# Kernel optimization log

Hardware: AMD Instinct MI355X
Metric: run time of the kernel (lower is better)

Reference implementation:

```python
import jax, jax.numpy as jnp
import numpy as np

B, S, D = 4, 4096, 1024

def setup_inputs() -> dict:
    key = jax.random.key(0)
    ks = jax.random.split(key, 7)
    scale = 1.0 / np.sqrt(D)
    X  = jax.random.normal(ks[0], (B, S, D), dtype=jnp.float32)
    Wq = jax.random.normal(ks[1], (D, D), dtype=jnp.float32) * scale
    bq = jnp.zeros((D,), dtype=jnp.float32)
    Wk = jax.random.normal(ks[2], (D, D), dtype=jnp.float32) * scale
    bk = jnp.zeros((D,), dtype=jnp.float32)
    Wv = jax.random.normal(ks[3], (D, D), dtype=jnp.float32) * scale
    bv = jnp.zeros((D,), dtype=jnp.float32)
    return {"X": X, "Wq": Wq, "bq": bq, "Wk": Wk, "bk": bk, "Wv": Wv, "bv": bv}

def reference(X, Wq, bq, Wk, bk, Wv, bv):
    # Linear projections (torch Linear: x @ W.T + b; here W stored as [D_in, D_out])
    Q = jnp.einsum('bsd,de->bse', X, Wq) + bq
    K = jnp.einsum('bsd,de->bse', X, Wk) + bk
    V = jnp.einsum('bsd,de->bse', X, Wv) + bv
    inv_sqrt_d = 1.0 / jnp.sqrt(jnp.float32(X.shape[-1]))
    scores = jnp.einsum('bqd,bkd->bqk', Q, K) * inv_sqrt_d  # [B,S,S]
    weights = jax.nn.sigmoid(scores)  # elementwise, no row normalization
    return jnp.einsum('bqk,bkd->bqd', weights, V)
```

## Files before the change

kernel.cpp:

```cpp
#include <hip/hip_runtime.h>
#include <hip/hip_bf16.h>

typedef __bf16 bf16_t;
typedef bf16_t bf16x8 __attribute__((ext_vector_type(8)));
typedef float f32x4 __attribute__((ext_vector_type(4)));

constexpr int D_DIM = 1024;
constexpr int S_DIM = 4096;
constexpr int B_DIM = 4;

__global__ void cast_f32_bf16(const float* __restrict__ in, bf16_t* __restrict__ out) {
  size_t i = ((size_t)blockIdx.x * blockDim.x + threadIdx.x) * 8;
  float4 a = *(const float4*)(in + i);
  float4 b = *(const float4*)(in + i + 4);
  bf16x8 o;
  o[0] = (bf16_t)a.x; o[1] = (bf16_t)a.y; o[2] = (bf16_t)a.z; o[3] = (bf16_t)a.w;
  o[4] = (bf16_t)b.x; o[5] = (bf16_t)b.y; o[6] = (bf16_t)b.z; o[7] = (bf16_t)b.w;
  *(bf16x8*)(out + i) = o;
}

__global__ void transpose_cast_1024(const float* __restrict__ in, bf16_t* __restrict__ out) {
  __shared__ float t[32][33];
  int x0 = blockIdx.x * 32, y0 = blockIdx.y * 32;
#pragma unroll
  for (int i = 0; i < 32; i += 8)
    t[threadIdx.y + i][threadIdx.x] =
        in[(size_t)(y0 + threadIdx.y + i) * D_DIM + (x0 + threadIdx.x)];
  __syncthreads();
#pragma unroll
  for (int i = 0; i < 32; i += 8)
    out[(size_t)(x0 + threadIdx.y + i) * D_DIM + (y0 + threadIdx.x)] =
        (bf16_t)t[threadIdx.x][threadIdx.y + i];
}

constexpr int BM2 = 256, BN2 = 256;

#define VMCNT4 asm volatile("s_waitcnt vmcnt(4)" ::: "memory")
#define VMCNT0 asm volatile("s_waitcnt vmcnt(0)" ::: "memory")
#define CFENCE asm volatile("" ::: "memory")
#define BAR __builtin_amdgcn_s_barrier()
#define PRIO1 __builtin_amdgcn_s_setprio(1)
#define PRIO0 __builtin_amdgcn_s_setprio(0)

__device__ __forceinline__ void stage_half(const bf16_t* __restrict__ g, int ld,
                                           char* lds, int tid) {
  const int w = tid >> 6, l = tid & 63;
  const int rw = l >> 3;
  const int gl = (l & 7) ^ rw;
  char* l0 = lds + w * 1024;
  const bf16_t* s0 = g + (size_t)(w * 8 + rw) * ld + gl * 8;
  __builtin_amdgcn_global_load_lds((const __attribute__((address_space(1))) void*)s0,
                                   (__attribute__((address_space(3))) void*)l0, 16, 0, 0);
  __builtin_amdgcn_global_load_lds(
      (const __attribute__((address_space(1))) void*)(s0 + (size_t)64 * ld),
      (__attribute__((address_space(3))) void*)(l0 + 8192), 16, 0, 0);
}

__device__ __forceinline__ void load_a4(const char* __restrict__ At, int wr, int fm, int s,
                                        int kxa, int kxb, bf16x8 (&af)[4][2]) {
#pragma unroll
  for (int m = 0; m < 4; ++m) {
    const char* p = At + (wr + (s * 4 + m) * 16 + fm) * 128;
    af[m][0] = *(const bf16x8*)(p + kxa);
    af[m][1] = *(const bf16x8*)(p + kxb);
  }
}

__device__ __forceinline__ void load_b8(const char* __restrict__ Bt_, int wc, int fm,
                                        int kxa, int kxb, bf16x8 (&bfr)[4][2]) {
#pragma unroll
  for (int n = 0; n < 4; ++n) {
    const char* p = Bt_ + (wc + n * 16 + fm) * 128;
    bfr[n][0] = *(const bf16x8*)(p + kxa);
    bfr[n][1] = *(const bf16x8*)(p + kxb);
  }
}

__device__ __forceinline__ void mfma_q(f32x4 (&acc)[8][4], const bf16x8 (&af)[4][2],
                                       const bf16x8 (&bfr)[4][2], int ms, int ns) {
#pragma unroll
  for (int kh = 0; kh < 2; ++kh)
#pragma unroll
    for (int m = 0; m < 4; ++m)
#pragma unroll
      for (int n = 0; n < 2; ++n)
        acc[ms * 4 + m][ns * 2 + n] = __builtin_amdgcn_mfma_f32_16x16x32_bf16(
            af[m][kh], bfr[ns * 2 + n][kh], acc[ms * 4 + m][ns * 2 + n], 0, 0, 0);
}

template <int EPI, bool SWAP>
__global__ __launch_bounds__(512, 2) void gemm256(
    const bf16_t* __restrict__ A, const bf16_t* __restrict__ Bt,
    void* __restrict__ C0, void* __restrict__ C1, void* __restrict__ C2,
    const float* __restrict__ b0, const float* __restrict__ b1, const float* __restrict__ b2,
    int K, int lda, int ldb, int ldc, float scale,
    size_t sA, size_t sB, size_t sC) {
  __shared__ __align__(16) char smem[131072];
  char* const A0t = smem;
  char* const B0t = smem + 32768;
  char* const A1t = smem + 65536;
  char* const B1t = smem + 98304;

  const int tid = threadIdx.x;
  const int lane = tid & 63;
  const int w = tid >> 6;
  const int wr = (w >> 2) * 128;
  const int wc = (w & 3) * 64;
  const int fm = lane & 15;
  const int ssw = (fm & 7) << 4;
  const int kp = (lane >> 4) << 4;
  const int kxa = kp ^ ssw;
  const int kxb = (64 | kp) ^ ssw;

  const int nx = gridDim.x, ny = gridDim.y;
  const int nwg = nx * ny * gridDim.z;
  const int flat = blockIdx.x + nx * (blockIdx.y + ny * blockIdx.z);
  const int q = nwg >> 3;
  const int L = (flat & 7) * q + (flat >> 3);
  const int lx = L % nx;
  const int lt = L / nx;
  const int ly = lt % ny;
  const int lz = lt / ny;

  const int bx = SWAP ? ly : lx;
  const int by = SWAP ? lx : ly;

  const bf16_t* Ag = A + (size_t)lz * sA + (size_t)by * BM2 * lda;
  const bf16_t* Bg = Bt + (size_t)lz * sB + (size_t)bx * BN2 * ldb;

  f32x4 acc[8][4] = {};
  bf16x8 af[4][2], bfr[4][2];

  const int NI = K / 128;

  stage_half(Ag, lda, A0t, tid);
  stage_half(Ag + (size_t)128 * lda, lda, A0t + 16384, tid);
  stage_half(Bg, ldb, B0t, tid);
  stage_half(Bg + (size_t)128 * ldb, ldb, B0t + 16384, tid);
  stage_half(Bg + 64, ldb, B1t, tid);
  stage_half(Bg + 64 + (size_t)128 * ldb, ldb, B1t + 16384, tid);
  VMCNT4;
  BAR;

  for (int it = 0; it < NI; ++it) {
    const bool last = (it == NI - 1);
    const bf16_t* Ao  = Ag + (size_t)(2 * it + 1) * 64;
    const bf16_t* Ae2 = Ag + (size_t)(2 * it + 2) * 64;
    const bf16_t* Be2 = Bg + (size_t)(2 * it + 2) * 64;
    const bf16_t* Bo2 = Bg + (size_t)(2 * it + 3) * 64;

    load_a4(A0t, wr, fm, 0, kxa, kxb, af);
    load_b8(B0t, wc, fm, kxa, kxb, bfr);
    stage_half(Ao, lda, A1t, tid);
    CFENCE; BAR;
    PRIO1; mfma_q(acc, af, bfr, 0, 0); PRIO0;
    BAR;

    load_a4(A0t, wr, fm, 1, kxa, kxb, af);
    stage_half(Ao + (size_t)128 * lda, lda, A1t + 16384, tid);
    if (!last) stage_half(Be2, ldb, B0t, tid);
    CFENCE; BAR;
    PRIO1; mfma_q(acc, af, bfr, 1, 0); PRIO0;
    BAR;

    if (!last) stage_half(Be2 + (size_t)128 * ldb, ldb, B0t + 16384, tid);
    CFENCE; BAR;
    PRIO1; mfma_q(acc, af, bfr, 1, 1); PRIO0;
    BAR;

    load_a4(A0t, wr, fm, 0, kxa, kxb, af);
    CFENCE; BAR;
    PRIO1; mfma_q(acc, af, bfr, 0, 1); PRIO0;
    if (last) { VMCNT0; } else { VMCNT4; }
    BAR;

    load_a4(A1t, wr, fm, 0, kxa, kxb, af);
    load_b8(B1t, wc, fm, kxa, kxb, bfr);
    if (!last) stage_half(Ae2, lda, A0t, tid);
    CFENCE; BAR;
    PRIO1; mfma_q(acc, af, bfr, 0, 0); PRIO0;
    BAR;

    load_a4(A1t, wr, fm, 1, kxa, kxb, af);
    if (!last) stage_half(Ae2 + (size_t)128 * lda, lda, A0t + 16384, tid);
    CFENCE; BAR;
    PRIO1; mfma_q(acc, af, bfr, 1, 0); PRIO0;
    BAR;

    if (!last) stage_half(Bo2, ldb, B1t, tid);
    CFENCE; BAR;
    PRIO1; mfma_q(acc, af, bfr, 1, 1); PRIO0;
    BAR;

    load_a4(A1t, wr, fm, 0, kxa, kxb, af);
    if (!last) stage_half(Bo2 + (size_t)128 * ldb, ldb, B1t + 16384, tid);
    CFENCE; BAR;
    PRIO1; mfma_q(acc, af, bfr, 0, 1); PRIO0;
    if (!last) { VMCNT4; }
    BAR;
  }

  const int row0 = by * BM2 + wr + (lane >> 4) * 4;
  const int col0 = bx * BN2 + wc + fm;

  if constexpr (EPI == 0) {
    const int seg = bx >> 2;
    const float* bias = (seg == 0) ? b0 : (seg == 1) ? b1 : b2;
#pragma unroll
    for (int i = 0; i < 8; ++i) {
#pragma unroll
      for (int j = 0; j < 4; ++j) {
        const int n = col0 + j * 16;
        const int nl = n & 1023;
        const float bv = bias[nl];
#pragma unroll
        for (int r = 0; r < 4; ++r) {
          const int m = row0 + i * 16 + r;
          float v = acc[i][j][r] + bv;
          if (seg < 2) {
            bf16_t* C = (bf16_t*)(seg == 0 ? C0 : C1);
            C[(size_t)m * D_DIM + nl] = (bf16_t)v;
          } else {
            bf16_t* C = (bf16_t*)C2;
            C[((size_t)(m >> 12) << 22) + (size_t)nl * S_DIM + (m & (S_DIM - 1))] = (bf16_t)v;
          }
        }
      }
    }
  } else {
#pragma unroll
    for (int i = 0; i < 8; ++i) {
#pragma unroll
      for (int j = 0; j < 4; ++j) {
        const int n = col0 + j * 16;
#pragma unroll
        for (int r = 0; r < 4; ++r) {
          const int m = row0 + i * 16 + r;
          float v = acc[i][j][r];
          if constexpr (EPI == 2) {
            bf16_t* C = (bf16_t*)C0 + (size_t)lz * sC;
            float s = 1.0f / (1.0f + __expf(-v * scale));
            C[(size_t)m * ldc + n] = (bf16_t)s;
          } else {
            float* C = (float*)C0 + (size_t)lz * sC;
            C[(size_t)m * ldc + n] = v;
          }
        }
      }
    }
  }
}

extern "C" void kernel_launch(void* const* d_in, const int* in_sizes, int n_in,
                              void* d_out, int out_size, void* d_ws, size_t ws_size,
                              hipStream_t stream) {
  const float* X  = (const float*)d_in[0];
  const float* Wq = (const float*)d_in[1];
  const float* bq = (const float*)d_in[2];
  const float* Wk = (const float*)d_in[3];
  const float* bk = (const float*)d_in[4];
  const float* Wv = (const float*)d_in[5];
  const float* bv = (const float*)d_in[6];
  float* out = (float*)d_out;

  const int M = B_DIM * S_DIM;
  const size_t SD = (size_t)S_DIM * D_DIM;
  const size_t E  = (size_t)M * D_DIM;
  const size_t PE1 = (size_t)S_DIM * S_DIM;
  const size_t WE = (size_t)D_DIM * D_DIM;

  size_t need4 = (4 * PE1 + 3 * E + 3 * WE) * sizeof(bf16_t);
  const int PB = (ws_size >= need4) ? 4 : 1;
  const size_t psz = (size_t)PB * PE1;

  bf16_t* ws = (bf16_t*)d_ws;
  bf16_t* P   = ws;
  bf16_t* Xb  = ws;
  bf16_t* Qb  = ws + psz;
  bf16_t* Kb  = Qb + E;
  bf16_t* Vt  = Kb + E;
  bf16_t* Wt  = Vt + E;

  cast_f32_bf16<<<dim3((unsigned)(E / 8 / 256)), dim3(256), 0, stream>>>(X, Xb);

  dim3 tg(D_DIM / 32, D_DIM / 32), tb(32, 8);
  transpose_cast_1024<<<tg, tb, 0, stream>>>(Wq, Wt);
  transpose_cast_1024<<<tg, tb, 0, stream>>>(Wk, Wt + WE);
  transpose_cast_1024<<<tg, tb, 0, stream>>>(Wv, Wt + 2 * WE);

  dim3 pg(3 * D_DIM / BN2, M / BM2, 1);
  gemm256<0, false><<<pg, dim3(512), 0, stream>>>(
      Xb, Wt, Qb, Kb, Vt, bq, bk, bv, D_DIM, D_DIM, D_DIM, D_DIM, 1.0f, 0, 0, 0);

  const float scale = 0.03125f;
  for (int b0 = 0; b0 < B_DIM; b0 += PB) {
    dim3 sg(S_DIM / BN2, S_DIM / BM2, PB);
    gemm256<2, false><<<sg, dim3(512), 0, stream>>>(
        Qb + (size_t)b0 * SD, Kb + (size_t)b0 * SD, P,
        nullptr, nullptr, nullptr, nullptr, nullptr,
        D_DIM, D_DIM, D_DIM, S_DIM, scale, SD, SD, PE1);
    dim3 vg(S_DIM / BM2, D_DIM / BN2, PB);
    gemm256<3, true><<<vg, dim3(512), 0, stream>>>(
        P, Vt + (size_t)b0 * SD, out + (size_t)b0 * SD,
        nullptr, nullptr, nullptr, nullptr, nullptr,
        S_DIM, S_DIM, S_DIM, D_DIM, 1.0f, PE1, SD, SD);
  }
}
```

Measured before the change: 557.8 us.

## Split B fragment loads and reschedule global-to-LDS stages with explicit lgkmcnt waits

Splits the B-fragment LDS read into two halves loaded just before the MFMA quarters that use them. The global-to-LDS stage issues for the next B and A tiles move to different sub-steps, and the vmcnt threshold changes to match. Explicit lgkmcnt waits and sched_barriers are added so LDS reads complete and the compiler cannot reorder them around the MFMA blocks. The aim is better overlap of LDS reads, global loads and MFMA work with lower register pressure, at the risk of introducing hazards if the reordered stage writes collide with pending reads.

```diff
diff --git a/kernel.cpp b/kernel.cpp
--- a/kernel.cpp
+++ b/kernel.cpp
@@ -36,7 +36,11 @@
 constexpr int BM2 = 256, BN2 = 256;
 
 #define VMCNT4 asm volatile("s_waitcnt vmcnt(4)" ::: "memory")
+#define VMCNT2 asm volatile("s_waitcnt vmcnt(2)" ::: "memory")
 #define VMCNT0 asm volatile("s_waitcnt vmcnt(0)" ::: "memory")
+#define LGKM8  asm volatile("s_waitcnt lgkmcnt(8)" ::: "memory")
+#define LGKM0  asm volatile("s_waitcnt lgkmcnt(0)" ::: "memory")
+#define SCHEDB __builtin_amdgcn_sched_barrier(0)
 #define CFENCE asm volatile("" ::: "memory")
 #define BAR __builtin_amdgcn_s_barrier()
 #define PRIO1 __builtin_amdgcn_s_setprio(1)
@@ -66,10 +70,10 @@
   }
 }
 
-__device__ __forceinline__ void load_b8(const char* __restrict__ Bt_, int wc, int fm,
+__device__ __forceinline__ void load_b2(const char* __restrict__ Bt_, int wc, int fm, int n0,
                                         int kxa, int kxb, bf16x8 (&bfr)[4][2]) {
 #pragma unroll
-  for (int n = 0; n < 4; ++n) {
+  for (int n = n0; n < n0 + 2; ++n) {
     const char* p = Bt_ + (wc + n * 16 + fm) * 128;
     bfr[n][0] = *(const bf16x8*)(p + kxa);
     bfr[n][1] = *(const bf16x8*)(p + kxb);
@@ -150,51 +154,65 @@
     const bf16_t* Bo2 = Bg + (size_t)(2 * it + 3) * 64;
 
     load_a4(A0t, wr, fm, 0, kxa, kxb, af);
-    load_b8(B0t, wc, fm, kxa, kxb, bfr);
+    load_b2(B0t, wc, fm, 0, kxa, kxb, bfr);
     stage_half(Ao, lda, A1t, tid);
-    CFENCE; BAR;
+    LGKM8; CFENCE; BAR;
+    LGKM0; SCHEDB;
     PRIO1; mfma_q(acc, af, bfr, 0, 0); PRIO0;
     BAR;
 
     load_a4(A0t, wr, fm, 1, kxa, kxb, af);
     stage_half(Ao + (size_t)128 * lda, lda, A1t + 16384, tid);
+    CFENCE; BAR;
+    LGKM0; SCHEDB;
+    PRIO1; mfma_q(acc, af, bfr, 1, 0); PRIO0;
+    BAR;
+
+    load_b2(B0t, wc, fm, 2, kxa, kxb, bfr);
+    CFENCE; BAR;
+    LGKM0; SCHEDB;
+    PRIO1; mfma_q(acc, af, bfr, 1, 1); PRIO0;
+    BAR;
+
+    load_a4(A0t, wr, fm, 0, kxa, kxb, af);
     if (!last) stage_half(Be2, ldb, B0t, tid);
     CFENCE; BAR;
-    PRIO1; mfma_q(acc, af, bfr, 1, 0); PRIO0;
-    BAR;
-
-    if (!last) stage_half(Be2 + (size_t)128 * ldb, ldb, B0t + 16384, tid);
-    CFENCE; BAR;
-    PRIO1; mfma_q(acc, af, bfr, 1, 1); PRIO0;
-    BAR;
-
-    load_a4(A0t, wr, fm, 0, kxa, kxb, af);
-    CFENCE; BAR;
+    LGKM0; SCHEDB;
     PRIO1; mfma_q(acc, af, bfr, 0, 1); PRIO0;
-    if (last) { VMCNT0; } else { VMCNT4; }
+    if (last) { VMCNT0; } else { VMCNT2; }
     BAR;
 
     load_a4(A1t, wr, fm, 0, kxa, kxb, af);
-    load_b8(B1t, wc, fm, kxa, kxb, bfr);
-    if (!last) stage_half(Ae2, lda, A0t, tid);
-    CFENCE; BAR;
+    load_b2(B1t, wc, fm, 0, kxa, kxb, bfr);
+    if (!last) {
+      stage_half(Be2 + (size_t)128 * ldb, ldb, B0t + 16384, tid);
+      stage_half(Ae2, lda, A0t, tid);
+    }
+    LGKM8; CFENCE; BAR;
+    LGKM0; SCHEDB;
     PRIO1; mfma_q(acc, af, bfr, 0, 0); PRIO0;
     BAR;
 
     load_a4(A1t, wr, fm, 1, kxa, kxb, af);
     if (!last) stage_half(Ae2 + (size_t)128 * lda, lda, A0t + 16384, tid);
     CFENCE; BAR;
+    LGKM0; SCHEDB;
     PRIO1; mfma_q(acc, af, bfr, 1, 0); PRIO0;
     BAR;
 
-    if (!last) stage_half(Bo2, ldb, B1t, tid);
-    CFENCE; BAR;
+    load_b2(B1t, wc, fm, 2, kxa, kxb, bfr);
+    CFENCE; BAR;
+    LGKM0; SCHEDB;
     PRIO1; mfma_q(acc, af, bfr, 1, 1); PRIO0;
     BAR;
 
     load_a4(A1t, wr, fm, 0, kxa, kxb, af);
-    if (!last) stage_half(Bo2 + (size_t)128 * ldb, ldb, B1t + 16384, tid);
-    CFENCE; BAR;
+    if (!last) {
+      stage_half(Bo2, ldb, B1t, tid);
+      stage_half(Bo2 + (size_t)128 * ldb, ldb, B1t + 16384, tid);
+    }
+    CFENCE; BAR;
+    LGKM0; SCHEDB;
     PRIO1; mfma_q(acc, af, bfr, 0, 1); PRIO0;
     if (!last) { VMCNT4; }
     BAR;
```

Result: faster. 535.6 us (-4.0%).
